# Optimization experiments

Measured on AMD Instinct MI355X. Metric: run time of the kernel, lower is better.

Reference implementation:

```python
import jax, jax.numpy as jnp
import numpy as np

FEATURES_DIM = 64 * (64 * 10 + 1)  # 41024


def setup_inputs() -> dict:
    key = jax.random.key(0)
    ks = jax.random.split(key, 11)
    def lin(k, out_d, in_d):
        bound = 1.0 / np.sqrt(in_d)
        kw, kb = jax.random.split(k)
        W = jax.random.uniform(kw, (out_d, in_d), jnp.float32, -bound, bound)
        b = jax.random.uniform(kb, (out_d,), jnp.float32, -bound, bound)
        return W, b
    x = jax.random.uniform(ks[0], (2 * FEATURES_DIM,), jnp.float32)
    W_my, b_my = lin(ks[1], 256, FEATURES_DIM)
    W_opp, b_opp = lin(ks[2], 256, FEATURES_DIM)
    W1, b1 = lin(ks[3], 32, 512)
    W2, b2 = lin(ks[4], 32, 32)
    W3, b3 = lin(ks[5], 1, 32)
    return {"x": x, "W_my": W_my, "b_my": b_my, "W_opp": W_opp, "b_opp": b_opp,
            "W1": W1, "b1": b1, "W2": W2, "b2": b2, "W3": W3, "b3": b3}


def reference(x, W_my, b_my, W_opp, b_opp, W1, b1, W2, b2, W3, b3):
    # HalfKP accumulators: two huge sparse-linear (here dense) 41024->256 + ReLU
    my = jax.nn.relu(W_my @ x[:FEATURES_DIM] + b_my)      # [256]
    opp = jax.nn.relu(W_opp @ x[FEATURES_DIM:] + b_opp)   # [256]
    h = jnp.concatenate([my, opp])                        # [512]
    # small trailing MLP 512->32->32->1
    h = jax.nn.relu(W1 @ h + b1)
    h = jax.nn.relu(W2 @ h + b2)
    return W3 @ h + b3                                    # [1]
```

## Files before the change

### kernel.cpp

```cpp
#include <hip/hip_runtime.h>

#define FEAT  41024
#define NF4   (FEAT / 4)
#define HALF4 (NF4 / 2)
#define NBLK  1024

__global__ __launch_bounds__(256) void halfkp_matvec_part(
    const float* __restrict__ x,
    const float* __restrict__ W_my,
    const float* __restrict__ W_opp,
    float* __restrict__ partial)
{
    const int b    = blockIdx.x;
    const int tid  = threadIdx.x;
    const int row  = b >> 1;
    const int half = b & 1;

    const float4* __restrict__ W4 =
        (const float4*)(row < 256 ? W_my : W_opp)
        + (size_t)(row & 255) * NF4 + (size_t)half * HALF4;
    const float4* __restrict__ x4 =
        (const float4*)x + (row < 256 ? 0 : NF4) + (size_t)half * HALF4;

    float a0 = 0.f, a1 = 0.f, a2 = 0.f, a3 = 0.f;
    int i = tid;
    #pragma unroll
    for (int k = 0; k < 5; ++k) {
        float4 w0 = W4[i      ]; float4 v0 = x4[i      ];
        float4 w1 = W4[i + 256]; float4 v1 = x4[i + 256];
        float4 w2 = W4[i + 512]; float4 v2 = x4[i + 512];
        float4 w3 = W4[i + 768]; float4 v3 = x4[i + 768];
        a0 += w0.x*v0.x + w0.y*v0.y + w0.z*v0.z + w0.w*v0.w;
        a1 += w1.x*v1.x + w1.y*v1.y + w1.z*v1.z + w1.w*v1.w;
        a2 += w2.x*v2.x + w2.y*v2.y + w2.z*v2.z + w2.w*v2.w;
        a3 += w3.x*v3.x + w3.y*v3.y + w3.z*v3.z + w3.w*v3.w;
        i += 1024;
    }
    if (tid < 8) {
        float4 w = W4[5120 + tid]; float4 v = x4[5120 + tid];
        a0 += w.x*v.x + w.y*v.y + w.z*v.z + w.w*v.w;
    }

    float acc = (a0 + a1) + (a2 + a3);
    #pragma unroll
    for (int off = 32; off > 0; off >>= 1)
        acc += __shfl_down(acc, off, 64);

    __shared__ float red[4];
    if ((tid & 63) == 0) red[tid >> 6] = acc;
    __syncthreads();
    if (tid == 0)
        partial[b] = red[0] + red[1] + red[2] + red[3];
}

__global__ __launch_bounds__(1024) void mlp_head(
    const float* __restrict__ partial,
    const float* __restrict__ b_my, const float* __restrict__ b_opp,
    const float* __restrict__ W1,  const float* __restrict__ b1,
    const float* __restrict__ W2,  const float* __restrict__ b2,
    const float* __restrict__ W3,  const float* __restrict__ b3,
    float* __restrict__ out)
{
    __shared__ float hs[512];
    __shared__ float h1[32];
    __shared__ float h2[32];

    const int tid = threadIdx.x;
    const int o = tid >> 5;
    const int j = tid & 31;

    float w[16];
    #pragma unroll
    for (int k = 0; k < 16; ++k)
        w[k] = W1[o * 512 + j + 32 * k];

    if (tid < 512) {
        float p0 = partial[2 * tid];
        float p1 = partial[2 * tid + 1];
        float bias = (tid < 256) ? b_my[tid] : b_opp[tid - 256];
        float s = p0 + p1 + bias;
        hs[tid] = s > 0.f ? s : 0.f;
    }
    __syncthreads();

    float acc = 0.f;
    #pragma unroll
    for (int k = 0; k < 16; ++k)
        acc += w[k] * hs[j + 32 * k];
    acc += __shfl_down(acc, 16, 32);
    acc += __shfl_down(acc,  8, 32);
    acc += __shfl_down(acc,  4, 32);
    acc += __shfl_down(acc,  2, 32);
    acc += __shfl_down(acc,  1, 32);
    if (j == 0) {
        float s = acc + b1[o];
        h1[o] = s > 0.f ? s : 0.f;
    }
    __syncthreads();

    if (tid < 32) {
        float s = b2[tid];
        #pragma unroll 8
        for (int k = 0; k < 32; ++k)
            s += W2[tid * 32 + k] * h1[k];
        h2[tid] = s > 0.f ? s : 0.f;
    }
    __syncthreads();

    if (tid == 0) {
        float s = b3[0];
        #pragma unroll 8
        for (int k = 0; k < 32; ++k)
            s += W3[k] * h2[k];
        out[0] = s;
    }
}

extern "C" void kernel_launch(void* const* d_in, const int* in_sizes, int n_in,
                              void* d_out, int out_size, void* d_ws, size_t ws_size,
                              hipStream_t stream)
{
    const float* x     = (const float*)d_in[0];
    const float* W_my  = (const float*)d_in[1];
    const float* b_my  = (const float*)d_in[2];
    const float* W_opp = (const float*)d_in[3];
    const float* b_opp = (const float*)d_in[4];
    const float* W1    = (const float*)d_in[5];
    const float* b1    = (const float*)d_in[6];
    const float* W2    = (const float*)d_in[7];
    const float* b2    = (const float*)d_in[8];
    const float* W3    = (const float*)d_in[9];
    const float* b3    = (const float*)d_in[10];

    float* out     = (float*)d_out;
    float* partial = (float*)d_ws;

    halfkp_matvec_part<<<NBLK, 256, 0, stream>>>(x, W_my, W_opp, partial);
    mlp_head<<<1, 1024, 0, stream>>>(partial, b_my, b_opp,
                                     W1, b1, W2, b2, W3, b3, out);
}
```

Before: 22.42 us.

## Compute eight rows per block over column chunks to reuse x loads

Restructures the big matvec so each block handles 8 consecutive weight rows over one of 8 column chunks, loading each x vector once and reusing it for all 8 rows. Partial sums are written as 8 per row and reduced in the head kernel with float4 loads. This aims to cut redundant x traffic and increase independent loads in flight, at the cost of more registers and strided access across rows.

```diff
diff --git a/kernel.cpp b/kernel.cpp
--- a/kernel.cpp
+++ b/kernel.cpp
@@ -2,55 +2,68 @@
 
 #define FEAT  41024
 #define NF4   (FEAT / 4)
-#define HALF4 (NF4 / 2)
-#define NBLK  1024
+#define RPB   8
+#define NCH   8
+#define CF4   (NF4 / NCH)
+#define NBLK  ((512 / RPB) * NCH)
 
-__global__ __launch_bounds__(256) void halfkp_matvec_part(
+__global__ __launch_bounds__(256) void halfkp_rows(
     const float* __restrict__ x,
     const float* __restrict__ W_my,
     const float* __restrict__ W_opp,
     float* __restrict__ partial)
 {
-    const int b    = blockIdx.x;
-    const int tid  = threadIdx.x;
-    const int row  = b >> 1;
-    const int half = b & 1;
+    const int b     = blockIdx.x;
+    const int tid   = threadIdx.x;
+    const int group = b >> 3;
+    const int ch    = b & 7;
+    const int row0  = group * RPB;
 
-    const float4* __restrict__ W4 =
-        (const float4*)(row < 256 ? W_my : W_opp)
-        + (size_t)(row & 255) * NF4 + (size_t)half * HALF4;
-    const float4* __restrict__ x4 =
-        (const float4*)x + (row < 256 ? 0 : NF4) + (size_t)half * HALF4;
+    const float4* __restrict__ Wb =
+        (const float4*)(row0 < 256 ? W_my : W_opp)
+        + (size_t)(row0 & 255) * NF4 + (size_t)ch * CF4;
+    const float4* __restrict__ xb =
+        (const float4*)x + (row0 < 256 ? 0 : NF4) + (size_t)ch * CF4;
 
-    float a0 = 0.f, a1 = 0.f, a2 = 0.f, a3 = 0.f;
-    int i = tid;
+    float acc[RPB];
+    #pragma unroll
+    for (int r = 0; r < RPB; ++r) acc[r] = 0.f;
+
     #pragma unroll
     for (int k = 0; k < 5; ++k) {
-        float4 w0 = W4[i      ]; float4 v0 = x4[i      ];
-        float4 w1 = W4[i + 256]; float4 v1 = x4[i + 256];
-        float4 w2 = W4[i + 512]; float4 v2 = x4[i + 512];
-        float4 w3 = W4[i + 768]; float4 v3 = x4[i + 768];
-        a0 += w0.x*v0.x + w0.y*v0.y + w0.z*v0.z + w0.w*v0.w;
-        a1 += w1.x*v1.x + w1.y*v1.y + w1.z*v1.z + w1.w*v1.w;
-        a2 += w2.x*v2.x + w2.y*v2.y + w2.z*v2.z + w2.w*v2.w;
-        a3 += w3.x*v3.x + w3.y*v3.y + w3.z*v3.z + w3.w*v3.w;
-        i += 1024;
+        const int i = tid + k * 256;
+        float4 xv = xb[i];
+        #pragma unroll
+        for (int r = 0; r < RPB; ++r) {
+            float4 w = Wb[(size_t)r * NF4 + i];
+            acc[r] += w.x*xv.x + w.y*xv.y + w.z*xv.z + w.w*xv.w;
+        }
     }
-    if (tid < 8) {
-        float4 w = W4[5120 + tid]; float4 v = x4[5120 + tid];
-        a0 += w.x*v.x + w.y*v.y + w.z*v.z + w.w*v.w;
+    if (tid < 2) {
+        const int i = 1280 + tid;
+        float4 xv = xb[i];
+        #pragma unroll
+        for (int r = 0; r < RPB; ++r) {
+            float4 w = Wb[(size_t)r * NF4 + i];
+            acc[r] += w.x*xv.x + w.y*xv.y + w.z*xv.z + w.w*xv.w;
+        }
     }
 
-    float acc = (a0 + a1) + (a2 + a3);
     #pragma unroll
-    for (int off = 32; off > 0; off >>= 1)
-        acc += __shfl_down(acc, off, 64);
-
-    __shared__ float red[4];
-    if ((tid & 63) == 0) red[tid >> 6] = acc;
+    for (int r = 0; r < RPB; ++r) {
+        #pragma unroll
+        for (int off = 32; off > 0; off >>= 1)
+            acc[r] += __shfl_down(acc[r], off, 64);
+    }
+    __shared__ float red[4][RPB];
+    if ((tid & 63) == 0) {
+        #pragma unroll
+        for (int r = 0; r < RPB; ++r) red[tid >> 6][r] = acc[r];
+    }
     __syncthreads();
-    if (tid == 0)
-        partial[b] = red[0] + red[1] + red[2] + red[3];
+    if (tid < RPB)
+        partial[(size_t)(row0 + tid) * NCH + ch] =
+            (red[0][tid] + red[1][tid]) + (red[2][tid] + red[3][tid]);
 }
 
 __global__ __launch_bounds__(1024) void mlp_head(
@@ -75,10 +88,11 @@
         w[k] = W1[o * 512 + j + 32 * k];
 
     if (tid < 512) {
-        float p0 = partial[2 * tid];
-        float p1 = partial[2 * tid + 1];
+        const float4* p4 = (const float4*)(partial + (size_t)tid * NCH);
+        float4 pa = p4[0], pb = p4[1];
         float bias = (tid < 256) ? b_my[tid] : b_opp[tid - 256];
-        float s = p0 + p1 + bias;
+        float s = ((pa.x + pa.y) + (pa.z + pa.w))
+                + ((pb.x + pb.y) + (pb.z + pb.w)) + bias;
         hs[tid] = s > 0.f ? s : 0.f;
     }
     __syncthreads();
@@ -135,7 +149,7 @@
     float* out     = (float*)d_out;
     float* partial = (float*)d_ws;
 
-    halfkp_matvec_part<<<NBLK, 256, 0, stream>>>(x, W_my, W_opp, partial);
+    halfkp_rows<<<NBLK, 256, 0, stream>>>(x, W_my, W_opp, partial);
     mlp_head<<<1, 1024, 0, stream>>>(partial, b_my, b_opp,
                                      W1, b1, W2, b2, W3, b3, out);
 }
```

New measurement: 22.74 us. Within noise of the previous version (+1.4%).
